# Performance work log

Hardware: AMD Instinct MI355X
Metric: run time of the kernel (lower is better)

## Reference

```python
import jax, jax.numpy as jnp
import numpy as np

N, M, DIM_K, DIM_V = 8192, 8192, 256, 256

def setup_inputs() -> dict:
    key = jax.random.key(0)
    kq, kk, kv = jax.random.split(key, 3)
    Q = jax.random.normal(kq, (N, DIM_K), dtype=jnp.float32)
    K = jax.random.normal(kk, (M, DIM_K), dtype=jnp.float32)
    V = jax.random.normal(kv, (M, DIM_V), dtype=jnp.float32)
    return {"Q": Q, "K": K, "V": V}

def reference(Q, K, V):
    # scores: [N, M] = Q @ K^T / sqrt(dim_k)
    scale = 1.0 / jnp.sqrt(jnp.asarray(Q.shape[-1], dtype=Q.dtype))
    scores = jnp.einsum('nd,md->nm', Q, K) * scale
    attn = jax.nn.softmax(scores, axis=-1)  # softmax over keys
    return attn @ V  # [N, dim_v]
```

## Files before the change

### kernel.cpp

```cpp
#include <hip/hip_runtime.h>
#include <hip/hip_bf16.h>
#include <hip/hip_fp16.h>


typedef __attribute__((ext_vector_type(16))) float floatx16;
typedef __attribute__((ext_vector_type(8)))  short short8;

union S8u { short8 v; unsigned short u[8]; };

#if __has_builtin(__builtin_amdgcn_exp2f)
#define EXP2F(x) __builtin_amdgcn_exp2f(x)
#else
#define EXP2F(x) exp2f(x)
#endif

__device__ __forceinline__ unsigned short f2bf(float f) {
    unsigned int u = __builtin_bit_cast(unsigned int, f);
    unsigned int r = u + 0x7fffu + ((u >> 16) & 1u);
    return (unsigned short)(r >> 16);
}

__device__ __forceinline__ unsigned cvtpk_bf16(float lo, float hi) {
    unsigned r;
    asm("v_cvt_pk_bf16_f32 %0, %1, %2" : "=v"(r) : "v"(lo), "v"(hi));
    return r;
}

__device__ __forceinline__ void gload16(const void* g, void* l) {
    __builtin_amdgcn_global_load_lds(
        (const __attribute__((address_space(1))) unsigned int*)g,
        (__attribute__((address_space(3))) unsigned int*)l, 16, 0, 0);
}


__global__ void cvt_bf16_kernel(const float* __restrict__ in,
                                unsigned short* __restrict__ out,
                                float scale, int n8) {
    int i = blockIdx.x * blockDim.x + threadIdx.x;
    if (i >= n8) return;
    const float4* p = reinterpret_cast<const float4*>(in) + (size_t)i * 2;
    float4 a = p[0], b = p[1];
    S8u r;
    r.u[0] = f2bf(a.x * scale); r.u[1] = f2bf(a.y * scale);
    r.u[2] = f2bf(a.z * scale); r.u[3] = f2bf(a.w * scale);
    r.u[4] = f2bf(b.x * scale); r.u[5] = f2bf(b.y * scale);
    r.u[6] = f2bf(b.z * scale); r.u[7] = f2bf(b.w * scale);
    *reinterpret_cast<short8*>(out + (size_t)i * 8) = r.v;
}

__global__ void transpose_v_kernel(const float* __restrict__ V,
                                   unsigned short* __restrict__ Vt) {
    __shared__ unsigned short T[64][72];
    const int kv0 = blockIdx.x * 64;
    const int v0  = blockIdx.y * 64;
    const int tid = threadIdx.x;
#pragma unroll
    for (int it = 0; it < 4; ++it) {
        int flat = it * 256 + tid;
        int r  = flat >> 4;
        int c4 = (flat & 15) * 4;
        float4 f = *reinterpret_cast<const float4*>(
            V + (size_t)(kv0 + r) * 256 + v0 + c4);
        T[c4 + 0][r] = f2bf(f.x);
        T[c4 + 1][r] = f2bf(f.y);
        T[c4 + 2][r] = f2bf(f.z);
        T[c4 + 3][r] = f2bf(f.w);
    }
    __syncthreads();
#pragma unroll
    for (int it = 0; it < 2; ++it) {
        int flat = it * 256 + tid;
        int r  = flat >> 3;
        int c8 = (flat & 7) * 8;
        short8 v8 = *reinterpret_cast<const short8*>(&T[r][c8]);
        *reinterpret_cast<short8*>(Vt + (size_t)(v0 + r) * 8192 + kv0 + c8) = v8;
    }
}


#define MFMA_B16 __builtin_amdgcn_mfma_f32_32x32x16_bf16

__global__ __launch_bounds__(256, 2)
void attn_kernel(const float* __restrict__ Qf,
                 const unsigned short* __restrict__ Kb,
                 const unsigned short* __restrict__ VtG,
                 __half* __restrict__ Opart,
                 float* __restrict__ Ml,
                 int kv_span, int gshift) {
    __shared__ __align__(16) unsigned char kbuf[2][16384];
    __shared__ __align__(16) unsigned char vbuf[2][16384];

    const int tid  = threadIdx.x;
    const int lane = tid & 63;
    const int w    = tid >> 6;
    const int l31  = lane & 31;
    const int h    = lane >> 5;

    const int ngm1 = (1 << gshift) - 1;
    const int id   = blockIdx.x + 64 * blockIdx.y;
    const int g    = id & ngm1;
    const int qblk = id >> gshift;
    const int kv_begin = g * kv_span;
    const int tiles = kv_span >> 5;
    const int q0 = qblk * 128 + w * 32;

    const float qs = 0.09016844005556021f;
    short8 qf[16];
    {
        const float* qp = Qf + (size_t)(q0 + l31) * 256 + h * 8;
#pragma unroll
        for (int ds = 0; ds < 16; ++ds) {
            float4 f0 = *reinterpret_cast<const float4*>(qp + ds * 16);
            float4 f1 = *reinterpret_cast<const float4*>(qp + ds * 16 + 4);
            uint4 uu;
            uu.x = cvtpk_bf16(f0.x * qs, f0.y * qs);
            uu.y = cvtpk_bf16(f0.z * qs, f0.w * qs);
            uu.z = cvtpk_bf16(f1.x * qs, f1.y * qs);
            uu.w = cvtpk_bf16(f1.z * qs, f1.w * qs);
            qf[ds] = __builtin_bit_cast(short8, uu);
        }
    }

    floatx16 o[8];
#pragma unroll
    for (int vt = 0; vt < 8; ++vt)
#pragma unroll
        for (int r = 0; r < 16; ++r) o[vt][r] = 0.f;
    float m_run = -1e30f, l_run = 0.f;

    int offk[4], offv[4];
#pragma unroll
    for (int i = 0; i < 4; ++i) {
        int j  = i * 256 + tid;
        int rk = j >> 5, ck = (j & 31) ^ (rk & 7);
        offk[i] = rk * 256 + ck * 8;
        int rv = j >> 2, cv = (j & 3) ^ ((rv >> 1) & 3);
        offv[i] = rv * 8192 + cv * 8;
    }

    auto STAGEK = [&](int kv0, int bufsel) {
        const unsigned short* ks = Kb + (size_t)kv0 * 256;
#pragma unroll
        for (int i = 0; i < 4; ++i)
            gload16(ks + offk[i], &kbuf[bufsel][(i * 256 + w * 64) * 16]);
    };
    auto STAGEV = [&](int kv0, int bufsel) {
        const unsigned short* vs = VtG + kv0;
#pragma unroll
        for (int i = 0; i < 4; ++i)
            gload16(vs + offv[i], &vbuf[bufsel][(i * 256 + w * 64) * 16]);
    };

    STAGEK(kv_begin, 0);
    STAGEV(kv_begin, 0);
    asm volatile("s_waitcnt vmcnt(4)" ::: "memory");
    __builtin_amdgcn_s_barrier();

    const int swz  = l31 & 7;
    const int vswz = (l31 >> 1) & 3;

    auto buildPA = [&](const floatx16& sv, int rbase) -> short8 {
        unsigned cpk0 = cvtpk_bf16(sv[rbase + 0], sv[rbase + 1]);
        unsigned cpk1 = cvtpk_bf16(sv[rbase + 2], sv[rbase + 3]);
        unsigned cpk2 = cvtpk_bf16(sv[rbase + 4], sv[rbase + 5]);
        unsigned cpk3 = cvtpk_bf16(sv[rbase + 6], sv[rbase + 7]);
        uint4 uu;
#if __has_builtin(__builtin_amdgcn_permlane32_swap)
        auto r02 = __builtin_amdgcn_permlane32_swap((int)cpk0, (int)cpk2, false, false);
        auto r13 = __builtin_amdgcn_permlane32_swap((int)cpk1, (int)cpk3, false, false);
        uu.x = (unsigned)r02[0]; uu.y = (unsigned)r13[0];
        uu.z = (unsigned)r02[1]; uu.w = (unsigned)r13[1];
#else
        unsigned send0 = h ? cpk0 : cpk2;
        unsigned send1 = h ? cpk1 : cpk3;
        unsigned r0 = (unsigned)__shfl_xor((int)send0, 32);
        unsigned r1 = (unsigned)__shfl_xor((int)send1, 32);
        uu.x = h ? r0 : cpk0;
        uu.y = h ? r1 : cpk1;
        uu.z = h ? cpk2 : r0;
        uu.w = h ? cpk3 : r1;
#endif
        return __builtin_bit_cast(short8, uu);
    };

    for (int t = 0; t < tiles; ++t) {
        const int cur = t & 1;
        const int nxt = cur ^ 1;
        const int tn  = (t + 1 < tiles) ? t + 1 : t;

        STAGEK(kv_begin + tn * 32, nxt);

        const unsigned char* kl = kbuf[cur];
        floatx16 sA, sB;
#pragma unroll
        for (int r = 0; r < 16; ++r) { sA[r] = 0.f; sB[r] = 0.f; }
        __builtin_amdgcn_s_setprio(1);
#pragma unroll
        for (int ds = 0; ds < 8; ++ds) {
            int c0 = (ds * 2 + h) ^ swz;
            short8 a0 = *reinterpret_cast<const short8*>(
                kl + (size_t)l31 * 512 + c0 * 16);
            sA = MFMA_B16(a0, qf[ds], sA, 0, 0, 0);
        }
#pragma unroll
        for (int ds = 8; ds < 16; ++ds) {
            int c0 = (ds * 2 + h) ^ swz;
            short8 a0 = *reinterpret_cast<const short8*>(
                kl + (size_t)l31 * 512 + c0 * 16);
            sB = MFMA_B16(a0, qf[ds], sB, 0, 0, 0);
        }
        __builtin_amdgcn_s_setprio(0);
        floatx16 s0;
#pragma unroll
        for (int r = 0; r < 16; ++r) s0[r] = sA[r] + sB[r];

        {
            float t4[4];
#pragma unroll
            for (int i = 0; i < 4; ++i)
                t4[i] = fmaxf(fmaxf(s0[i], s0[i + 4]),
                              fmaxf(s0[i + 8], s0[i + 12]));
            float mt = fmaxf(fmaxf(t4[0], t4[1]), fmaxf(t4[2], t4[3]));
            mt = fmaxf(mt, __shfl_xor(mt, 32));
            if (__any(mt > m_run + 11.5f)) {
                float mnew = fmaxf(m_run, mt);
                float al = EXP2F(m_run - mnew);
                m_run = mnew;
                l_run *= al;
#pragma unroll
                for (int reg = 0; reg < 16; ++reg) {
                    int srcl = ((reg & 3) + 8 * (reg >> 2)) + 4 * h;
                    float alr = __shfl(al, srcl);
#pragma unroll
                    for (int vt = 0; vt < 8; ++vt) o[vt][reg] *= alr;
                }
            }
#pragma unroll
            for (int r = 0; r < 16; ++r) s0[r] = EXP2F(s0[r] - m_run);
            float u[4];
#pragma unroll
            for (int i = 0; i < 4; ++i)
                u[i] = (s0[i] + s0[i + 4]) + (s0[i + 8] + s0[i + 12]);
            float lt = (u[0] + u[1]) + (u[2] + u[3]);
            lt += __shfl_xor(lt, 32);
            l_run += lt;
        }

        asm volatile("s_waitcnt vmcnt(4)" ::: "memory");
        __builtin_amdgcn_s_barrier();

        STAGEV(kv_begin + tn * 32, nxt);

        const unsigned char* vl = vbuf[cur];
        __builtin_amdgcn_s_setprio(1);
#pragma unroll
        for (int kk = 0; kk < 2; ++kk) {
            short8 pa = buildPA(s0, kk * 8);
            int cvs = (kk * 2 + h) ^ vswz;
#pragma unroll
            for (int vt = 0; vt < 8; ++vt) {
                short8 b = *reinterpret_cast<const short8*>(
                    vl + (size_t)(vt * 32 + l31) * 64 + cvs * 16);
                o[vt] = MFMA_B16(pa, b, o[vt], 0, 0, 0);
            }
        }
        __builtin_amdgcn_s_setprio(0);

        asm volatile("s_waitcnt vmcnt(4)" ::: "memory");
        __builtin_amdgcn_s_barrier();
    }

    const size_t gq = (size_t)g * 8192;
    float linv = 1.0f / l_run;
#pragma unroll
    for (int reg = 0; reg < 16; ++reg) {
        int row = (reg & 3) + 8 * (reg >> 2) + 4 * h;
        float li = __shfl(linv, row);
#pragma unroll
        for (int vt = 0; vt < 8; ++vt)
            Opart[(gq + q0 + row) * 256 + vt * 32 + l31] =
                __float2half_rn(o[vt][reg] * li);
    }
    if (h == 0) {
        size_t idx = (gq + q0 + l31) * 2;
        Ml[idx]     = m_run;
        Ml[idx + 1] = l_run;
    }
}


__global__ void merge_kernel(const __half* __restrict__ Opart,
                             const float* __restrict__ Ml,
                             float* __restrict__ out, int ngroups) {
    int row = blockIdx.x;
    int col = threadIdx.x;
    float m = -1e30f;
    for (int g = 0; g < ngroups; ++g)
        m = fmaxf(m, Ml[((size_t)g * 8192 + row) * 2]);
    float den = 0.f, acc = 0.f;
    for (int g = 0; g < ngroups; ++g) {
        float wg = EXP2F(Ml[((size_t)g * 8192 + row) * 2] - m) *
                   Ml[((size_t)g * 8192 + row) * 2 + 1];
        den += wg;
        acc += wg * __half2float(Opart[((size_t)g * 8192 + row) * 256 + col]);
    }
    out[(size_t)row * 256 + col] = acc / den;
}


extern "C" void kernel_launch(void* const* d_in, const int* in_sizes, int n_in,
                              void* d_out, int out_size, void* d_ws, size_t ws_size,
                              hipStream_t stream) {
    const float* Q = (const float*)d_in[0];
    const float* K = (const float*)d_in[1];
    const float* V = (const float*)d_in[2];
    float* out = (float*)d_out;

    unsigned short* Kb = (unsigned short*)d_ws;
    unsigned short* Vt = Kb + (size_t)8192 * 256;

    const size_t base = (size_t)8192 * 256 * 2 * 2;
    const size_t osz  = (size_t)8192 * 256 * 2;
    const size_t mlsz = (size_t)8192 * 2 * 4;

    int gshift = 3;
    for (; gshift > 0; --gshift)
        if (base + ((osz + mlsz) << gshift) <= ws_size) break;
    int ng = 1 << gshift;

    __half* Opart = (__half*)((char*)d_ws + base);
    float*  Mlp   = (float*)((char*)d_ws + base + osz * (size_t)ng);

    const int n8 = 8192 * 256 / 8;
    cvt_bf16_kernel<<<n8 / 256, 256, 0, stream>>>(K, Kb, 1.0f, n8);
    transpose_v_kernel<<<dim3(128, 4), 256, 0, stream>>>(V, Vt);
    attn_kernel<<<dim3(64, ng), 256, 0, stream>>>(Q, Kb, Vt, Opart, Mlp,
                                                  8192 / ng, gshift);
    merge_kernel<<<8192, 256, 0, stream>>>(Opart, Mlp, out, ng);
}
```

Baseline: 135.3 us.

## Switch attention kernel to 16x16x32 MFMA with 64-row query blocks

Rewrites the attention kernel to use 16x16x32 bf16 MFMA instead of 32x32x16. Each wave now owns 16 query rows, so a block covers 64 rows and the grid doubles. The V tile loses its double buffer and is loaded at the start of each iteration with a full vmcnt(0) wait, which frees LDS and registers so occupancy can rise from 2 to 3 blocks. In exchange, K and V tiles are reused across half as many query rows, the P operand needs more cross-lane shuffles, and V loads are no longer prefetched a tile ahead.

```diff
diff --git a/kernel.cpp b/kernel.cpp
--- a/kernel.cpp
+++ b/kernel.cpp
@@ -3,7 +3,7 @@
 #include <hip/hip_fp16.h>
 
 
-typedef __attribute__((ext_vector_type(16))) float floatx16;
+typedef __attribute__((ext_vector_type(4)))  float floatx4;
 typedef __attribute__((ext_vector_type(8)))  short short8;
 
 union S8u { short8 v; unsigned short u[8]; };
@@ -78,9 +78,9 @@
 }
 
 
-#define MFMA_B16 __builtin_amdgcn_mfma_f32_32x32x16_bf16
-
-__global__ __launch_bounds__(256, 2)
+#define MFMA16 __builtin_amdgcn_mfma_f32_16x16x32_bf16
+
+__global__ __launch_bounds__(256, 3)
 void attn_kernel(const float* __restrict__ Qf,
                  const unsigned short* __restrict__ Kb,
                  const unsigned short* __restrict__ VtG,
@@ -88,30 +88,30 @@
                  float* __restrict__ Ml,
                  int kv_span, int gshift) {
     __shared__ __align__(16) unsigned char kbuf[2][16384];
-    __shared__ __align__(16) unsigned char vbuf[2][16384];
+    __shared__ __align__(16) unsigned char vbuf[16384];
 
     const int tid  = threadIdx.x;
     const int lane = tid & 63;
     const int w    = tid >> 6;
-    const int l31  = lane & 31;
-    const int h    = lane >> 5;
+    const int l15  = lane & 15;
+    const int lg   = lane >> 4;
 
     const int ngm1 = (1 << gshift) - 1;
-    const int id   = blockIdx.x + 64 * blockIdx.y;
+    const int id   = blockIdx.x + 128 * blockIdx.y;
     const int g    = id & ngm1;
     const int qblk = id >> gshift;
     const int kv_begin = g * kv_span;
     const int tiles = kv_span >> 5;
-    const int q0 = qblk * 128 + w * 32;
+    const int q0 = qblk * 64 + w * 16;
 
     const float qs = 0.09016844005556021f;
-    short8 qf[16];
+    short8 qf[8];
     {
-        const float* qp = Qf + (size_t)(q0 + l31) * 256 + h * 8;
-#pragma unroll
-        for (int ds = 0; ds < 16; ++ds) {
-            float4 f0 = *reinterpret_cast<const float4*>(qp + ds * 16);
-            float4 f1 = *reinterpret_cast<const float4*>(qp + ds * 16 + 4);
+        const float* qp = Qf + (size_t)(q0 + l15) * 256 + lg * 8;
+#pragma unroll
+        for (int ds = 0; ds < 8; ++ds) {
+            float4 f0 = *reinterpret_cast<const float4*>(qp + ds * 32);
+            float4 f1 = *reinterpret_cast<const float4*>(qp + ds * 32 + 4);
             uint4 uu;
             uu.x = cvtpk_bf16(f0.x * qs, f0.y * qs);
             uu.y = cvtpk_bf16(f0.z * qs, f0.w * qs);
@@ -121,11 +121,9 @@
         }
     }
 
-    floatx16 o[8];
-#pragma unroll
-    for (int vt = 0; vt < 8; ++vt)
-#pragma unroll
-        for (int r = 0; r < 16; ++r) o[vt][r] = 0.f;
+    floatx4 o[16];
+#pragma unroll
+    for (int vt = 0; vt < 16; ++vt) o[vt] = floatx4{0.f, 0.f, 0.f, 0.f};
     float m_run = -1e30f, l_run = 0.f;
 
     int offk[4], offv[4];
@@ -144,83 +142,51 @@
         for (int i = 0; i < 4; ++i)
             gload16(ks + offk[i], &kbuf[bufsel][(i * 256 + w * 64) * 16]);
     };
-    auto STAGEV = [&](int kv0, int bufsel) {
+    auto STAGEV = [&](int kv0) {
         const unsigned short* vs = VtG + kv0;
 #pragma unroll
         for (int i = 0; i < 4; ++i)
-            gload16(vs + offv[i], &vbuf[bufsel][(i * 256 + w * 64) * 16]);
+            gload16(vs + offv[i], &vbuf[(i * 256 + w * 64) * 16]);
     };
 
     STAGEK(kv_begin, 0);
-    STAGEV(kv_begin, 0);
-    asm volatile("s_waitcnt vmcnt(4)" ::: "memory");
+    asm volatile("s_waitcnt vmcnt(0)" ::: "memory");
     __builtin_amdgcn_s_barrier();
 
-    const int swz  = l31 & 7;
-    const int vswz = (l31 >> 1) & 3;
-
-    auto buildPA = [&](const floatx16& sv, int rbase) -> short8 {
-        unsigned cpk0 = cvtpk_bf16(sv[rbase + 0], sv[rbase + 1]);
-        unsigned cpk1 = cvtpk_bf16(sv[rbase + 2], sv[rbase + 3]);
-        unsigned cpk2 = cvtpk_bf16(sv[rbase + 4], sv[rbase + 5]);
-        unsigned cpk3 = cvtpk_bf16(sv[rbase + 6], sv[rbase + 7]);
-        uint4 uu;
-#if __has_builtin(__builtin_amdgcn_permlane32_swap)
-        auto r02 = __builtin_amdgcn_permlane32_swap((int)cpk0, (int)cpk2, false, false);
-        auto r13 = __builtin_amdgcn_permlane32_swap((int)cpk1, (int)cpk3, false, false);
-        uu.x = (unsigned)r02[0]; uu.y = (unsigned)r13[0];
-        uu.z = (unsigned)r02[1]; uu.w = (unsigned)r13[1];
-#else
-        unsigned send0 = h ? cpk0 : cpk2;
-        unsigned send1 = h ? cpk1 : cpk3;
-        unsigned r0 = (unsigned)__shfl_xor((int)send0, 32);
-        unsigned r1 = (unsigned)__shfl_xor((int)send1, 32);
-        uu.x = h ? r0 : cpk0;
-        uu.y = h ? r1 : cpk1;
-        uu.z = h ? cpk2 : r0;
-        uu.w = h ? cpk3 : r1;
-#endif
-        return __builtin_bit_cast(short8, uu);
-    };
+    const int swzK = l15 & 7;
+    const int vswz = (l15 >> 1) & 3;
+    const int src1 = l15 + (((lg << 1) & 3) << 4);
+    const int src2 = l15 + ((((lg << 1) + 1) & 3) << 4);
 
     for (int t = 0; t < tiles; ++t) {
         const int cur = t & 1;
         const int nxt = cur ^ 1;
         const int tn  = (t + 1 < tiles) ? t + 1 : t;
 
+        STAGEV(kv_begin + t * 32);
         STAGEK(kv_begin + tn * 32, nxt);
 
         const unsigned char* kl = kbuf[cur];
-        floatx16 sA, sB;
-#pragma unroll
-        for (int r = 0; r < 16; ++r) { sA[r] = 0.f; sB[r] = 0.f; }
+        floatx4 sA = floatx4{0.f, 0.f, 0.f, 0.f};
+        floatx4 sB = floatx4{0.f, 0.f, 0.f, 0.f};
         __builtin_amdgcn_s_setprio(1);
 #pragma unroll
         for (int ds = 0; ds < 8; ++ds) {
-            int c0 = (ds * 2 + h) ^ swz;
-            short8 a0 = *reinterpret_cast<const short8*>(
-                kl + (size_t)l31 * 512 + c0 * 16);
-            sA = MFMA_B16(a0, qf[ds], sA, 0, 0, 0);
-        }
-#pragma unroll
-        for (int ds = 8; ds < 16; ++ds) {
-            int c0 = (ds * 2 + h) ^ swz;
-            short8 a0 = *reinterpret_cast<const short8*>(
-                kl + (size_t)l31 * 512 + c0 * 16);
-            sB = MFMA_B16(a0, qf[ds], sB, 0, 0, 0);
+            int c0 = (ds * 4 + lg) ^ swzK;
+            short8 aA = *reinterpret_cast<const short8*>(
+                kl + (size_t)l15 * 512 + c0 * 16);
+            short8 aB = *reinterpret_cast<const short8*>(
+                kl + (size_t)(l15 + 16) * 512 + c0 * 16);
+            sA = MFMA16(aA, qf[ds], sA, 0, 0, 0);
+            sB = MFMA16(aB, qf[ds], sB, 0, 0, 0);
         }
         __builtin_amdgcn_s_setprio(0);
-        floatx16 s0;
-#pragma unroll
-        for (int r = 0; r < 16; ++r) s0[r] = sA[r] + sB[r];
 
         {
-            float t4[4];
-#pragma unroll
-            for (int i = 0; i < 4; ++i)
-                t4[i] = fmaxf(fmaxf(s0[i], s0[i + 4]),
-                              fmaxf(s0[i + 8], s0[i + 12]));
-            float mt = fmaxf(fmaxf(t4[0], t4[1]), fmaxf(t4[2], t4[3]));
+            float m0 = fmaxf(fmaxf(sA[0], sA[1]), fmaxf(sA[2], sA[3]));
+            float m1 = fmaxf(fmaxf(sB[0], sB[1]), fmaxf(sB[2], sB[3]));
+            float mt = fmaxf(m0, m1);
+            mt = fmaxf(mt, __shfl_xor(mt, 16));
             mt = fmaxf(mt, __shfl_xor(mt, 32));
             if (__any(mt > m_run + 11.5f)) {
                 float mnew = fmaxf(m_run, mt);
@@ -228,61 +194,75 @@
                 m_run = mnew;
                 l_run *= al;
 #pragma unroll
-                for (int reg = 0; reg < 16; ++reg) {
-                    int srcl = ((reg & 3) + 8 * (reg >> 2)) + 4 * h;
-                    float alr = __shfl(al, srcl);
-#pragma unroll
-                    for (int vt = 0; vt < 8; ++vt) o[vt][reg] *= alr;
+                for (int r = 0; r < 4; ++r) {
+                    float alr = __shfl(al, lg * 4 + r);
+#pragma unroll
+                    for (int vt = 0; vt < 16; ++vt) o[vt][r] *= alr;
                 }
             }
 #pragma unroll
-            for (int r = 0; r < 16; ++r) s0[r] = EXP2F(s0[r] - m_run);
-            float u[4];
-#pragma unroll
-            for (int i = 0; i < 4; ++i)
-                u[i] = (s0[i] + s0[i + 4]) + (s0[i + 8] + s0[i + 12]);
-            float lt = (u[0] + u[1]) + (u[2] + u[3]);
+            for (int r = 0; r < 4; ++r) sA[r] = EXP2F(sA[r] - m_run);
+#pragma unroll
+            for (int r = 0; r < 4; ++r) sB[r] = EXP2F(sB[r] - m_run);
+            float lt = ((sA[0] + sA[1]) + (sA[2] + sA[3])) +
+                       ((sB[0] + sB[1]) + (sB[2] + sB[3]));
+            lt += __shfl_xor(lt, 16);
             lt += __shfl_xor(lt, 32);
             l_run += lt;
         }
 
+        short8 pa;
+        {
+            unsigned a0 = cvtpk_bf16(sA[0], sA[1]);
+            unsigned a1 = cvtpk_bf16(sA[2], sA[3]);
+            unsigned b0 = cvtpk_bf16(sB[0], sB[1]);
+            unsigned b1 = cvtpk_bf16(sB[2], sB[3]);
+            unsigned x0 = (unsigned)__shfl((int)a0, src1);
+            unsigned y0 = (unsigned)__shfl((int)b0, src1);
+            unsigned x1 = (unsigned)__shfl((int)a1, src1);
+            unsigned y1 = (unsigned)__shfl((int)b1, src1);
+            unsigned x2 = (unsigned)__shfl((int)a0, src2);
+            unsigned y2 = (unsigned)__shfl((int)b0, src2);
+            unsigned x3 = (unsigned)__shfl((int)a1, src2);
+            unsigned y3 = (unsigned)__shfl((int)b1, src2);
+            uint4 uu;
+            uu.x = (lg < 2) ? x0 : y0;
+            uu.y = (lg < 2) ? x1 : y1;
+            uu.z = (lg < 2) ? x2 : y2;
+            uu.w = (lg < 2) ? x3 : y3;
+            pa = __builtin_bit_cast(short8, uu);
+        }
+
         asm volatile("s_waitcnt vmcnt(4)" ::: "memory");
         __builtin_amdgcn_s_barrier();
 
-        STAGEV(kv_begin + tn * 32, nxt);
-
-        const unsigned char* vl = vbuf[cur];
         __builtin_amdgcn_s_setprio(1);
 #pragma unroll
-        for (int kk = 0; kk < 2; ++kk) {
-            short8 pa = buildPA(s0, kk * 8);
-            int cvs = (kk * 2 + h) ^ vswz;
-#pragma unroll
-            for (int vt = 0; vt < 8; ++vt) {
-                short8 b = *reinterpret_cast<const short8*>(
-                    vl + (size_t)(vt * 32 + l31) * 64 + cvs * 16);
-                o[vt] = MFMA_B16(pa, b, o[vt], 0, 0, 0);
-            }
+        for (int vt = 0; vt < 16; ++vt) {
+            int cv = lg ^ vswz;
+            short8 b = *reinterpret_cast<const short8*>(
+                &vbuf[(size_t)(vt * 16 + l15) * 64 + cv * 16]);
+            o[vt] = MFMA16(pa, b, o[vt], 0, 0, 0);
         }
         __builtin_amdgcn_s_setprio(0);
 
-        asm volatile("s_waitcnt vmcnt(4)" ::: "memory");
+        asm volatile("s_waitcnt vmcnt(0)" ::: "memory");
         __builtin_amdgcn_s_barrier();
     }
 
     const size_t gq = (size_t)g * 8192;
     float linv = 1.0f / l_run;
 #pragma unroll
-    for (int reg = 0; reg < 16; ++reg) {
-        int row = (reg & 3) + 8 * (reg >> 2) + 4 * h;
+    for (int r = 0; r < 4; ++r) {
+        int row = lg * 4 + r;
         float li = __shfl(linv, row);
 #pragma unroll
-        for (int vt = 0; vt < 8; ++vt)
-            Opart[(gq + q0 + row) * 256 + vt * 32 + l31] =
-                __float2half_rn(o[vt][reg] * li);
-    }
-    if (h == 0) {
-        size_t idx = (gq + q0 + l31) * 2;
+        for (int vt = 0; vt < 16; ++vt)
+            Opart[(gq + q0 + row) * 256 + vt * 16 + l15] =
+                __float2half_rn(o[vt][r] * li);
+    }
+    if (lg == 0) {
+        size_t idx = (gq + q0 + l15) * 2;
         Ml[idx]     = m_run;
         Ml[idx + 1] = l_run;
     }
@@ -334,7 +314,7 @@
     const int n8 = 8192 * 256 / 8;
     cvt_bf16_kernel<<<n8 / 256, 256, 0, stream>>>(K, Kb, 1.0f, n8);
     transpose_v_kernel<<<dim3(128, 4), 256, 0, stream>>>(V, Vt);
-    attn_kernel<<<dim3(64, ng), 256, 0, stream>>>(Q, Kb, Vt, Opart, Mlp,
-                                                  8192 / ng, gshift);
+    attn_kernel<<<dim3(128, ng), 256, 0, stream>>>(Q, Kb, Vt, Opart, Mlp,
+                                                   8192 / ng, gshift);
     merge_kernel<<<8192, 256, 0, stream>>>(Opart, Mlp, out, ng);
 }
```

Measured after the change: 159.3 us. 1.18x slower.
